# Kernel optimization log

Hardware: AMD Instinct MI355X
Metric: run time of the kernel (lower is better)

Reference implementation:

```python
import jax, jax.numpy as jnp
import numpy as np

DIM = 384
HEADS = 12
WS = 7


def setup_inputs() -> dict:
    key = jax.random.key(0)
    ks = jax.random.split(key, 5)
    B, H, W = 16, 56, 56
    x = jax.random.normal(ks[0], (B, H * W, DIM), dtype=jnp.float32)
    # torch Linear weight (out,in) used as x @ W here, qkv_bias=False
    w_qkv = jax.random.normal(ks[1], (DIM, 3 * DIM), dtype=jnp.float32) * 0.02
    w_proj = jax.random.normal(ks[2], (DIM, DIM), dtype=jnp.float32) * 0.02
    b_proj = jax.random.normal(ks[3], (DIM,), dtype=jnp.float32) * 0.02
    # depthwise 3x3 conv (groups=dim): HWIO kernel (3,3,1,DIM), bias=True
    w_conv = jax.random.normal(ks[4], (3, 3, 1, DIM), dtype=jnp.float32) * 0.02
    b_conv = jnp.zeros((DIM,), jnp.float32)
    return {"x": x, "w_qkv": w_qkv, "w_proj": w_proj, "b_proj": b_proj,
            "w_conv": w_conv, "b_conv": b_conv, "H": H, "W": W}


def reference(x, w_qkv, w_proj, b_proj, w_conv, b_conv, H, W):
    B, N, C = x.shape
    hd = C // HEADS
    scale = hd ** (-0.5)
    hg, wg = H // WS, W // WS  # H,W chosen divisible by ws (no-pad fast path)

    qkv = x @ w_qkv  # (B, N, 3C)
    q, k, v = jnp.split(qkv, 3, axis=-1)

    def to_win(t):
        # (B,N,C) -> (B, n_windows, heads, ws*ws, head_dim)
        t = t.reshape(B, hg, WS, wg, WS, HEADS, hd)
        return t.transpose(0, 1, 3, 5, 2, 4, 6).reshape(B, hg * wg, HEADS, WS * WS, hd)

    qw, kw, vw = to_win(q), to_win(k), to_win(v)

    attn = jax.nn.softmax(jnp.einsum('bwhqd,bwhkd->bwhqk', qw, kw) * scale, axis=-1)
    out = jnp.einsum('bwhqk,bwhkd->bwhqd', attn, vw)
    # merge windows back: (B,nw,heads,q,d) -> (B,N,C)
    out = out.reshape(B, hg, wg, HEADS, WS, WS, hd)
    out = out.transpose(0, 1, 4, 2, 5, 3, 6).reshape(B, N, C)

    # LIM: win2img(img2win(v)) is just v as (B,C,H,W); depthwise 3x3 conv
    v_img = v.reshape(B, H, W, C).transpose(0, 3, 1, 2)
    v_lim = jax.lax.conv_general_dilated(
        v_img, w_conv, window_strides=(1, 1), padding='SAME',
        dimension_numbers=('NCHW', 'HWIO', 'NCHW'), feature_group_count=C)
    v_lim = v_lim + b_conv[None, :, None, None]
    v_lim = v_lim.reshape(B, C, N).transpose(0, 2, 1)  # (B, N, C)

    out = out + v_lim
    return out @ w_proj + b_proj
```

## Files before the change

### kernel.cpp

```cpp
#include <hip/hip_runtime.h>
#include <cstdint>
#include <cstddef>

typedef __bf16 bf16x8 __attribute__((ext_vector_type(8)));
typedef float floatx4 __attribute__((ext_vector_type(4)));

#define DEV static __device__ __forceinline__

DEV float bf2f(uint16_t u) {
    union { uint32_t i; float f; } x; x.i = ((uint32_t)u) << 16; return x.f;
}
DEV uint16_t f2bf(float f) {
    uint32_t u = __float_as_uint(f);
    uint32_t r = (u + 0x7FFFu + ((u >> 16) & 1u)) >> 16;
    return (uint16_t)r;
}
DEV bf16x8 as_bf8(uint4 u) {
    union { uint4 u; bf16x8 b; } c; c.u = u; return c.b;
}
DEV void g2l16(const void* g, void* l) {
    __builtin_amdgcn_global_load_lds(
        (const __attribute__((address_space(1))) void*)g,
        (__attribute__((address_space(3))) void*)l, 16, 0, 0);
}

union U16x8 { uint16_t h[8]; uint4 u; };

constexpr int DIMC  = 384;
constexpr int HEADS = 12;
constexpr int IMH   = 56, IMW = 56;
constexpr int NTOK  = IMH * IMW;
constexpr int BATCH = 16;
constexpr int MTOT  = BATCH * NTOK;
constexpr int QKVLD = 3 * DIMC;
constexpr int GK    = 384;

__global__ __launch_bounds__(256) void cvt_bf16(const float* __restrict__ in,
                                                uint16_t* __restrict__ out)
{
    size_t i = ((size_t)blockIdx.x * 256 + threadIdx.x) * 8;
    float4 a = *(const float4*)(in + i);
    float4 b = *(const float4*)(in + i + 4);
    U16x8 t;
    t.h[0] = f2bf(a.x); t.h[1] = f2bf(a.y); t.h[2] = f2bf(a.z); t.h[3] = f2bf(a.w);
    t.h[4] = f2bf(b.x); t.h[5] = f2bf(b.y); t.h[6] = f2bf(b.z); t.h[7] = f2bf(b.w);
    *(uint4*)(out + i) = t.u;
}

__global__ __launch_bounds__(256) void transpose_cvt(const float* __restrict__ in,
                                                     uint16_t* __restrict__ out,
                                                     int R, int C)
{
    int idx = blockIdx.x * 256 + threadIdx.x;
    int r = idx % R, c = idx / R;
    out[idx] = f2bf(in[(size_t)r * C + c]);
}

template<bool CF32>
__global__ __launch_bounds__(256) void gemm_bt(const uint16_t* __restrict__ A,
                                               const uint16_t* __restrict__ Bt,
                                               const float* __restrict__ bias,
                                               void* __restrict__ Cptr,
                                               int N)
{
    __shared__ __align__(16) uint16_t sA[2][128 * 32];
    __shared__ __align__(16) uint16_t sB[2][128 * 32];

    const int t    = threadIdx.x;
    const int NB   = N >> 7;
    const int bid  = blockIdx.x;
    const int chunk = bid / (8 * NB);
    const int r     = bid % (8 * NB);
    const int bm    = chunk * 8 + (r & 7);
    const int bn    = r >> 3;
    const int wave = t >> 6, lane = t & 63;
    const int wm   = (wave >> 1) * 64, wn = (wave & 1) * 64;
    const int lr   = lane & 15, quad = lane >> 4;

    const uint16_t* Ag = A  + (size_t)(bm * 128 + (t >> 2)) * GK + (t & 3) * 8;
    const uint16_t* Bg = Bt + (size_t)(bn * 128 + (t >> 2)) * GK + (t & 3) * 8;

    auto stage = [&](int buf, int k0) {
        g2l16(Ag + k0, sA[buf] + wave * 512);
        g2l16(Ag + (size_t)64 * GK + k0, sA[buf] + 2048 + wave * 512);
        g2l16(Bg + k0, sB[buf] + wave * 512);
        g2l16(Bg + (size_t)64 * GK + k0, sB[buf] + 2048 + wave * 512);
    };

    floatx4 acc[4][4] = {};

    stage(0, 0);
    __syncthreads();

    #pragma unroll
    for (int ks = 0; ks < 12; ++ks) {
        const int cur = ks & 1;
        if (ks < 11) stage(cur ^ 1, (ks + 1) * 32);

        bf16x8 af[4], bfr[4];
        #pragma unroll
        for (int mt = 0; mt < 4; ++mt)
            af[mt] = *(const bf16x8*)&sA[cur][(wm + mt * 16 + lr) * 32 + quad * 8];
        #pragma unroll
        for (int nt = 0; nt < 4; ++nt)
            bfr[nt] = *(const bf16x8*)&sB[cur][(wn + nt * 16 + lr) * 32 + quad * 8];
        #pragma unroll
        for (int mt = 0; mt < 4; ++mt)
            #pragma unroll
            for (int nt = 0; nt < 4; ++nt)
                acc[mt][nt] = __builtin_amdgcn_mfma_f32_16x16x32_bf16(
                    af[mt], bfr[nt], acc[mt][nt], 0, 0, 0);

        __syncthreads();
    }

    #pragma unroll
    for (int mt = 0; mt < 4; ++mt) {
        #pragma unroll
        for (int nt = 0; nt < 4; ++nt) {
            int gc = bn * 128 + wn + nt * 16 + lr;
            float bv = bias ? bias[gc] : 0.0f;
            int gr0 = bm * 128 + wm + mt * 16 + quad * 4;
            #pragma unroll
            for (int i = 0; i < 4; ++i) {
                if constexpr (CF32) {
                    ((float*)Cptr)[(size_t)(gr0 + i) * N + gc] = acc[mt][nt][i] + bv;
                } else {
                    ((uint16_t*)Cptr)[(size_t)(gr0 + i) * N + gc] = f2bf(acc[mt][nt][i] + bv);
                }
            }
        }
    }
}

constexpr int PLD = 72;

__global__ __launch_bounds__(128) void attn_mfma(const uint16_t* __restrict__ qkv,
                                                 uint16_t* __restrict__ y)
{
    __shared__ uint16_t lds[2][(64 + 32) * PLD];

    const int wave = threadIdx.x >> 6;
    const int lane = threadIdx.x & 63;
    const int unit = blockIdx.x * 2 + wave;
    const int h  = unit % HEADS;
    const int w  = (unit / HEADS) & 63;
    const int b  = unit / (HEADS * 64);
    const int wy = w >> 3, wx = w & 7;
    const int lr = lane & 15, quad = lane >> 4;

    uint16_t* Pbuf = lds[wave];
    uint16_t* Vt   = lds[wave] + 64 * PLD;

    auto rowbase = [&](int i, int which) -> const uint16_t* {
        int py = i / 7, px = i % 7;
        int n = (wy * 7 + py) * IMW + wx * 7 + px;
        return qkv + (size_t)(b * NTOK + n) * QKVLD + which * DIMC + h * 32;
    };

    uint4 qf[4], kf[4];
    #pragma unroll
    for (int tm = 0; tm < 4; ++tm) {
        int i = tm * 16 + lr;
        if (i < 49) {
            qf[tm] = *(const uint4*)(rowbase(i, 0) + quad * 8);
            kf[tm] = *(const uint4*)(rowbase(i, 1) + quad * 8);
        } else {
            qf[tm] = uint4{0, 0, 0, 0};
            kf[tm] = uint4{0, 0, 0, 0};
        }
    }

    {
        int j = lane;
        uint16_t vrow[32];
        if (j < 49) {
            const uint16_t* vr = rowbase(j, 2);
            #pragma unroll
            for (int p = 0; p < 4; ++p) {
                U16x8 tmp; tmp.u = *(const uint4*)(vr + p * 8);
                #pragma unroll
                for (int q = 0; q < 8; ++q) vrow[p * 8 + q] = tmp.h[q];
            }
        } else {
            #pragma unroll
            for (int d = 0; d < 32; ++d) vrow[d] = 0;
        }
        #pragma unroll
        for (int d = 0; d < 32; ++d) Vt[d * PLD + j] = vrow[d];
    }

    floatx4 S[4][4] = {};
    #pragma unroll
    for (int tm = 0; tm < 4; ++tm)
        #pragma unroll
        for (int tn = 0; tn < 4; ++tn)
            S[tm][tn] = __builtin_amdgcn_mfma_f32_16x16x32_bf16(
                as_bf8(qf[tm]), as_bf8(kf[tn]), S[tm][tn], 0, 0, 0);

    const float scale = 0.17677669529663687f;
    const bool v3 = (lr == 0);
    #pragma unroll
    for (int tm = 0; tm < 4; ++tm) {
        #pragma unroll
        for (int i = 0; i < 4; ++i) {
            float e0 = __expf(S[tm][0][i] * scale);
            float e1 = __expf(S[tm][1][i] * scale);
            float e2 = __expf(S[tm][2][i] * scale);
            float e3 = v3 ? __expf(S[tm][3][i] * scale) : 0.0f;
            float s = e0 + e1 + e2 + e3;
            #pragma unroll
            for (int d = 1; d < 16; d <<= 1) s += __shfl_xor(s, d);
            float inv = 1.0f / s;
            int row = tm * 16 + quad * 4 + i;
            Pbuf[row * PLD + lr]      = f2bf(e0 * inv);
            Pbuf[row * PLD + 16 + lr] = f2bf(e1 * inv);
            Pbuf[row * PLD + 32 + lr] = f2bf(e2 * inv);
            Pbuf[row * PLD + 48 + lr] = f2bf(e3 * inv);
        }
    }

    floatx4 O[4][2] = {};
    #pragma unroll
    for (int kk = 0; kk < 2; ++kk) {
        bf16x8 pf[4], vf[2];
        #pragma unroll
        for (int tm = 0; tm < 4; ++tm)
            pf[tm] = *(const bf16x8*)&Pbuf[(tm * 16 + lr) * PLD + kk * 32 + quad * 8];
        #pragma unroll
        for (int tn = 0; tn < 2; ++tn)
            vf[tn] = *(const bf16x8*)&Vt[(tn * 16 + lr) * PLD + kk * 32 + quad * 8];
        #pragma unroll
        for (int tm = 0; tm < 4; ++tm)
            #pragma unroll
            for (int tn = 0; tn < 2; ++tn)
                O[tm][tn] = __builtin_amdgcn_mfma_f32_16x16x32_bf16(
                    pf[tm], vf[tn], O[tm][tn], 0, 0, 0);
    }

    #pragma unroll
    for (int tm = 0; tm < 4; ++tm) {
        #pragma unroll
        for (int i = 0; i < 4; ++i) {
            int r = tm * 16 + quad * 4 + i;
            if (r < 49) {
                int py = r / 7, px = r % 7;
                int n = (wy * 7 + py) * IMW + wx * 7 + px;
                uint16_t* dst = y + (size_t)(b * NTOK + n) * DIMC + h * 32;
                dst[lr]      = f2bf(O[tm][0][i]);
                dst[16 + lr] = f2bf(O[tm][1][i]);
            }
        }
    }
}

__global__ __launch_bounds__(256) void conv_kernel(const uint16_t* __restrict__ qkv,
                                                   const float* __restrict__ wconv,
                                                   const float* __restrict__ bconv,
                                                   uint16_t* __restrict__ y)
{
    constexpr int C8 = DIMC / 8;
    size_t idx = (size_t)blockIdx.x * 256 + threadIdx.x;
    int c8  = (int)(idx % C8);
    int rem = (int)(idx / C8);
    int n   = rem % NTOK;
    int b   = rem / NTOK;
    int c   = c8 * 8;
    int y0 = n / IMW, x0 = n % IMW;

    float acc[8];
    {
        float4 b0 = *(const float4*)(bconv + c);
        float4 b1 = *(const float4*)(bconv + c + 4);
        acc[0] = b0.x; acc[1] = b0.y; acc[2] = b0.z; acc[3] = b0.w;
        acc[4] = b1.x; acc[5] = b1.y; acc[6] = b1.z; acc[7] = b1.w;
    }

    const uint16_t* vbase = qkv + 2 * DIMC + c;
    #pragma unroll
    for (int ky = 0; ky < 3; ++ky) {
        int yy = y0 + ky - 1;
        if (yy < 0 || yy >= IMH) continue;
        #pragma unroll
        for (int kx = 0; kx < 3; ++kx) {
            int xx = x0 + kx - 1;
            if (xx < 0 || xx >= IMW) continue;
            U16x8 v;
            v.u = *(const uint4*)(vbase + (size_t)(b * NTOK + yy * IMW + xx) * QKVLD);
            const float* wp = wconv + (ky * 3 + kx) * DIMC + c;
            float4 w0 = *(const float4*)(wp);
            float4 w1 = *(const float4*)(wp + 4);
            acc[0] += bf2f(v.h[0]) * w0.x;
            acc[1] += bf2f(v.h[1]) * w0.y;
            acc[2] += bf2f(v.h[2]) * w0.z;
            acc[3] += bf2f(v.h[3]) * w0.w;
            acc[4] += bf2f(v.h[4]) * w1.x;
            acc[5] += bf2f(v.h[5]) * w1.y;
            acc[6] += bf2f(v.h[6]) * w1.z;
            acc[7] += bf2f(v.h[7]) * w1.w;
        }
    }

    uint16_t* yp = y + (size_t)rem * DIMC + c;
    U16x8 yo; yo.u = *(const uint4*)yp;
    #pragma unroll
    for (int j = 0; j < 8; ++j) yo.h[j] = f2bf(bf2f(yo.h[j]) + acc[j]);
    *(uint4*)yp = yo.u;
}

extern "C" void kernel_launch(void* const* d_in, const int* in_sizes, int n_in,
                              void* d_out, int out_size, void* d_ws, size_t ws_size,
                              hipStream_t stream)
{
    const float* x      = (const float*)d_in[0];
    const float* w_qkv  = (const float*)d_in[1];
    const float* w_proj = (const float*)d_in[2];
    const float* b_proj = (const float*)d_in[3];
    const float* w_conv = (const float*)d_in[4];
    const float* b_conv = (const float*)d_in[5];
    float* out = (float*)d_out;

    char* ws = (char*)d_ws;
    uint16_t* qkv    = (uint16_t*)ws;
    uint16_t* xb     = (uint16_t*)(ws + 115605504);
    uint16_t* yb     = xb;
    uint16_t* wqkvT  = (uint16_t*)(ws + 115605504 + 38535168);
    uint16_t* wprojT = wqkvT + QKVLD * GK;

    cvt_bf16<<<dim3((MTOT * DIMC) / (8 * 256)), 256, 0, stream>>>(x, xb);
    transpose_cvt<<<dim3((GK * QKVLD) / 256), 256, 0, stream>>>(w_qkv, wqkvT, GK, QKVLD);
    transpose_cvt<<<dim3((GK * DIMC) / 256), 256, 0, stream>>>(w_proj, wprojT, GK, DIMC);

    gemm_bt<false><<<dim3((MTOT / 128) * (QKVLD / 128)), 256, 0, stream>>>(
        xb, wqkvT, nullptr, qkv, QKVLD);

    attn_mfma<<<dim3(BATCH * 64 * HEADS / 2), 128, 0, stream>>>(qkv, yb);

    conv_kernel<<<dim3((MTOT * (DIMC / 8)) / 256), 256, 0, stream>>>(
        qkv, w_conv, b_conv, yb);

    gemm_bt<true><<<dim3((MTOT / 128) * (DIMC / 128)), 256, 0, stream>>>(
        yb, wprojT, b_proj, out, DIMC);
}
```

Measured before the change: 327.6 us.

## Fuse depthwise LIM conv into window attention kernel using LDS halo tile

Removes the separate depthwise 3x3 conv kernel and computes it inside the attention kernel. Each wave loads a 9x9 halo of V for its window and head into LDS, along with the conv weights and bias. The V transpose now reads from that halo, and the conv result is added to the attention output before the single write to y. This drops the read-modify-write of y and the second full read of V, at the cost of more LDS per block (which may lower occupancy) and the halo loads overlapping neighbouring windows. Rounding the conv result to bf16 before the add also changes numerics slightly.

Result: faster. 320.2 us (-2.3%).

```diff
diff --git a/kernel.cpp b/kernel.cpp
--- a/kernel.cpp
+++ b/kernel.cpp
@@ -134,11 +134,15 @@
 }
 
 constexpr int PLD = 72;
+constexpr int WAVE_ELEMS = (64 + 32) * PLD + 81 * 32;
 
 __global__ __launch_bounds__(128) void attn_mfma(const uint16_t* __restrict__ qkv,
+                                                 const float* __restrict__ wconv,
+                                                 const float* __restrict__ bconv,
                                                  uint16_t* __restrict__ y)
 {
-    __shared__ uint16_t lds[2][(64 + 32) * PLD];
+    __shared__ uint16_t lds[2][WAVE_ELEMS];
+    __shared__ float    warr_all[2][320];
 
     const int wave = threadIdx.x >> 6;
     const int lane = threadIdx.x & 63;
@@ -149,8 +153,32 @@
     const int wy = w >> 3, wx = w & 7;
     const int lr = lane & 15, quad = lane >> 4;
 
-    uint16_t* Pbuf = lds[wave];
-    uint16_t* Vt   = lds[wave] + 64 * PLD;
+    uint16_t* Pbuf  = lds[wave];
+    uint16_t* Vt    = lds[wave] + 64 * PLD;
+    uint16_t* Vhalo = lds[wave] + 96 * PLD;
+    float*    warr  = warr_all[wave];
+
+    #pragma unroll
+    for (int it = 0; it < 5; ++it) {
+        int idx = it * 64 + lane;
+        if (idx < 288) warr[idx] = wconv[(idx >> 5) * DIMC + h * 32 + (idx & 31)];
+    }
+    if (lane < 32) warr[288 + lane] = bconv[h * 32 + lane];
+
+    #pragma unroll
+    for (int it = 0; it < 6; ++it) {
+        int u = it * 16 + (lane >> 2);
+        int g = lane & 3;
+        if (u < 81) {
+            int hy = u / 9, hx = u % 9;
+            int iy = wy * 7 + hy - 1, ix = wx * 7 + hx - 1;
+            uint4 val{0, 0, 0, 0};
+            if (iy >= 0 && iy < IMH && ix >= 0 && ix < IMW)
+                val = *(const uint4*)(qkv + (size_t)(b * NTOK + iy * IMW + ix) * QKVLD
+                                      + 2 * DIMC + h * 32 + g * 8);
+            *(uint4*)&Vhalo[u * 32 + g * 8] = val;
+        }
+    }
 
     auto rowbase = [&](int i, int which) -> const uint16_t* {
         int py = i / 7, px = i % 7;
@@ -173,21 +201,18 @@
 
     {
         int j = lane;
-        uint16_t vrow[32];
         if (j < 49) {
-            const uint16_t* vr = rowbase(j, 2);
+            int hrow = (j / 7 + 1) * 9 + (j % 7 + 1);
             #pragma unroll
             for (int p = 0; p < 4; ++p) {
-                U16x8 tmp; tmp.u = *(const uint4*)(vr + p * 8);
+                U16x8 tmp; tmp.u = *(const uint4*)&Vhalo[hrow * 32 + p * 8];
                 #pragma unroll
-                for (int q = 0; q < 8; ++q) vrow[p * 8 + q] = tmp.h[q];
+                for (int q = 0; q < 8; ++q) Vt[(p * 8 + q) * PLD + j] = tmp.h[q];
             }
         } else {
             #pragma unroll
-            for (int d = 0; d < 32; ++d) vrow[d] = 0;
-        }
-        #pragma unroll
-        for (int d = 0; d < 32; ++d) Vt[d * PLD + j] = vrow[d];
+            for (int d = 0; d < 32; ++d) Vt[d * PLD + j] = 0;
+        }
     }
 
     floatx4 S[4][4] = {};
@@ -238,6 +263,46 @@
                     pf[tm], vf[tn], O[tm][tn], 0, 0, 0);
     }
 
+    uint16_t* convb = Vt;
+    #pragma unroll
+    for (int it = 0; it < 4; ++it) {
+        int u = it * 64 + lane;
+        if (u < 196) {
+            int j = u >> 2, g = u & 3;
+            int py = j / 7, px = j % 7;
+            float acc[8];
+            {
+                float4 b0 = *(const float4*)(warr + 288 + g * 8);
+                float4 b1 = *(const float4*)(warr + 288 + g * 8 + 4);
+                acc[0] = b0.x; acc[1] = b0.y; acc[2] = b0.z; acc[3] = b0.w;
+                acc[4] = b1.x; acc[5] = b1.y; acc[6] = b1.z; acc[7] = b1.w;
+            }
+            #pragma unroll
+            for (int ky = 0; ky < 3; ++ky) {
+                #pragma unroll
+                for (int kx = 0; kx < 3; ++kx) {
+                    int hrow = (py + ky) * 9 + (px + kx);
+                    U16x8 v; v.u = *(const uint4*)&Vhalo[hrow * 32 + g * 8];
+                    const float* wp = warr + (ky * 3 + kx) * 32 + g * 8;
+                    float4 w0 = *(const float4*)wp;
+                    float4 w1 = *(const float4*)(wp + 4);
+                    acc[0] += bf2f(v.h[0]) * w0.x;
+                    acc[1] += bf2f(v.h[1]) * w0.y;
+                    acc[2] += bf2f(v.h[2]) * w0.z;
+                    acc[3] += bf2f(v.h[3]) * w0.w;
+                    acc[4] += bf2f(v.h[4]) * w1.x;
+                    acc[5] += bf2f(v.h[5]) * w1.y;
+                    acc[6] += bf2f(v.h[6]) * w1.z;
+                    acc[7] += bf2f(v.h[7]) * w1.w;
+                }
+            }
+            U16x8 r;
+            #pragma unroll
+            for (int q = 0; q < 8; ++q) r.h[q] = f2bf(acc[q]);
+            *(uint4*)&convb[j * 32 + g * 8] = r.u;
+        }
+    }
+
     #pragma unroll
     for (int tm = 0; tm < 4; ++tm) {
         #pragma unroll
@@ -247,65 +312,13 @@
                 int py = r / 7, px = r % 7;
                 int n = (wy * 7 + py) * IMW + wx * 7 + px;
                 uint16_t* dst = y + (size_t)(b * NTOK + n) * DIMC + h * 32;
-                dst[lr]      = f2bf(O[tm][0][i]);
-                dst[16 + lr] = f2bf(O[tm][1][i]);
-            }
-        }
-    }
-}
-
-__global__ __launch_bounds__(256) void conv_kernel(const uint16_t* __restrict__ qkv,
-                                                   const float* __restrict__ wconv,
-                                                   const float* __restrict__ bconv,
-                                                   uint16_t* __restrict__ y)
-{
-    constexpr int C8 = DIMC / 8;
-    size_t idx = (size_t)blockIdx.x * 256 + threadIdx.x;
-    int c8  = (int)(idx % C8);
-    int rem = (int)(idx / C8);
-    int n   = rem % NTOK;
-    int b   = rem / NTOK;
-    int c   = c8 * 8;
-    int y0 = n / IMW, x0 = n % IMW;
-
-    float acc[8];
-    {
-        float4 b0 = *(const float4*)(bconv + c);
-        float4 b1 = *(const float4*)(bconv + c + 4);
-        acc[0] = b0.x; acc[1] = b0.y; acc[2] = b0.z; acc[3] = b0.w;
-        acc[4] = b1.x; acc[5] = b1.y; acc[6] = b1.z; acc[7] = b1.w;
-    }
-
-    const uint16_t* vbase = qkv + 2 * DIMC + c;
-    #pragma unroll
-    for (int ky = 0; ky < 3; ++ky) {
-        int yy = y0 + ky - 1;
-        if (yy < 0 || yy >= IMH) continue;
-        #pragma unroll
-        for (int kx = 0; kx < 3; ++kx) {
-            int xx = x0 + kx - 1;
-            if (xx < 0 || xx >= IMW) continue;
-            U16x8 v;
-            v.u = *(const uint4*)(vbase + (size_t)(b * NTOK + yy * IMW + xx) * QKVLD);
-            const float* wp = wconv + (ky * 3 + kx) * DIMC + c;
-            float4 w0 = *(const float4*)(wp);
-            float4 w1 = *(const float4*)(wp + 4);
-            acc[0] += bf2f(v.h[0]) * w0.x;
-            acc[1] += bf2f(v.h[1]) * w0.y;
-            acc[2] += bf2f(v.h[2]) * w0.z;
-            acc[3] += bf2f(v.h[3]) * w0.w;
-            acc[4] += bf2f(v.h[4]) * w1.x;
-            acc[5] += bf2f(v.h[5]) * w1.y;
-            acc[6] += bf2f(v.h[6]) * w1.z;
-            acc[7] += bf2f(v.h[7]) * w1.w;
-        }
-    }
-
-    uint16_t* yp = y + (size_t)rem * DIMC + c;
-    U16x8 yo; yo.u = *(const uint4*)yp;
-    #pragma unroll
-    for (int j = 0; j < 8; ++j) yo.h[j] = f2bf(bf2f(yo.h[j]) + acc[j]);
-    *(uint4*)yp = yo.u;
+                float c0 = bf2f(convb[r * 32 + lr]);
+                float c1 = bf2f(convb[r * 32 + 16 + lr]);
+                dst[lr]      = f2bf(O[tm][0][i] + c0);
+                dst[16 + lr] = f2bf(O[tm][1][i] + c1);
+            }
+        }
+    }
 }
 
 extern "C" void kernel_launch(void* const* d_in, const int* in_sizes, int n_in,
@@ -334,9 +347,7 @@
     gemm_bt<false><<<dim3((MTOT / 128) * (QKVLD / 128)), 256, 0, stream>>>(
         xb, wqkvT, nullptr, qkv, QKVLD);
 
-    attn_mfma<<<dim3(BATCH * 64 * HEADS / 2), 128, 0, stream>>>(qkv, yb);
-
-    conv_kernel<<<dim3((MTOT * (DIMC / 8)) / 256), 256, 0, stream>>>(
+    attn_mfma<<<dim3(BATCH * 64 * HEADS / 2), 128, 0, stream>>>(
         qkv, w_conv, b_conv, yb);
 
     gemm_bt<true><<<dim3((MTOT / 128) * (DIMC / 128)), 256, 0, stream>>>(
```
